# Kernel optimization log

Hardware: AMD Instinct MI355X
Metric: run time of the kernel (lower is better)

## Reference

```python
import jax, jax.numpy as jnp
import numpy as np

H = 256  # GRU hidden size


def _gru_scan(state, lengths, Wih, Whh, bih, bhh):
    # state: [B, T, D]; run a batched GRU over time, freezing h once t >= lengths[b]
    B, T, D = state.shape
    # precompute input gates for all timesteps: [T, B, 3H]
    gi_all = jnp.einsum('btd,gd->tbg', state, Wih) + bih

    def step(h, inp):
        gi, t = inp
        gh = h @ Whh.T + bhh                       # [B, 3H]
        i_r, i_z, i_n = jnp.split(gi, 3, axis=-1)
        h_r, h_z, h_n = jnp.split(gh, 3, axis=-1)
        r = jax.nn.sigmoid(i_r + h_r)
        z = jax.nn.sigmoid(i_z + h_z)
        n = jnp.tanh(i_n + r * h_n)
        h_new = (1.0 - z) * n + z * h              # torch GRUCell update
        mask = (t < lengths)[:, None]              # ragged: stop updating past length
        return jnp.where(mask, h_new, h), None

    h0 = jnp.zeros((B, H), state.dtype)
    h, _ = jax.lax.scan(step, h0, (gi_all, jnp.arange(T)))
    return h  # [B, H] = hidden after lengths[b] GRU steps


def _mlp(x, w1, b1, w2, b2, w3, b3, w4, b4, wq, bq):
    x = jax.nn.relu(x @ w1.T + b1)
    x = jax.nn.relu(x @ w2.T + b2)
    x = jax.nn.relu(x @ w3.T + b3)
    x = jax.nn.relu(x @ w4.T + b4)
    return x @ wq.T + bq  # [B, 1]


def setup_inputs() -> dict:
    key = jax.random.key(0)
    ks = jax.random.split(key, 40)
    B, T, D, A = 2048, 64, 15, 1
    inp = {}
    inp['state'] = jax.random.normal(ks[0], (B, T, D), jnp.float32)
    inp['action'] = jax.random.normal(ks[1], (B, A), jnp.float32)
    inp['lengths'] = jax.random.randint(ks[2], (B,), 1, T + 1, jnp.int32)
    i = 3
    for t in (1, 2):
        for name, shape, fan in [('Wih', (3 * H, D), D), ('Whh', (3 * H, H), H),
                                 ('bih', (3 * H,), H), ('bhh', (3 * H,), H)]:
            inp[f'g{t}_{name}'] = jax.random.normal(ks[i], shape, jnp.float32) / np.sqrt(fan)
            i += 1
        for name, (o, n) in [('fc1', (1024, H + D + A)), ('fc2', (1024, 1024)),
                             ('fc3', (512, 1024)), ('fc4', (256, 512)), ('q', (1, 256))]:
            inp[f'{name}_{t}_w'] = jax.random.normal(ks[i], (o, n), jnp.float32) / np.sqrt(n)
            i += 1
            inp[f'{name}_{t}_b'] = jax.random.normal(ks[i], (o,), jnp.float32) * 0.01
            i += 1
    return inp


def reference(state, action, lengths,
              g1_Wih, g1_Whh, g1_bih, g1_bhh,
              fc1_1_w, fc1_1_b, fc2_1_w, fc2_1_b, fc3_1_w, fc3_1_b,
              fc4_1_w, fc4_1_b, q_1_w, q_1_b,
              g2_Wih, g2_Whh, g2_bih, g2_bhh,
              fc1_2_w, fc1_2_b, fc2_2_w, fc2_2_b, fc3_2_w, fc3_2_b,
              fc4_2_w, fc4_2_b, q_2_w, q_2_b):
    h1 = _gru_scan(state, lengths, g1_Wih, g1_Whh, g1_bih, g1_bhh)
    h2 = _gru_scan(state, lengths, g2_Wih, g2_Whh, g2_bih, g2_bhh)
    aug = jnp.concatenate([state[:, 0, :], action], axis=-1)  # [B, 16]
    x1 = jnp.concatenate([aug, h1], axis=-1)                  # [B, 272]
    x2 = jnp.concatenate([aug, h2], axis=-1)
    out1 = _mlp(x1, fc1_1_w, fc1_1_b, fc2_1_w, fc2_1_b, fc3_1_w, fc3_1_b,
                fc4_1_w, fc4_1_b, q_1_w, q_1_b)
    out2 = _mlp(x2, fc1_2_w, fc1_2_b, fc2_2_w, fc2_2_b, fc3_2_w, fc3_2_b,
                fc4_2_w, fc4_2_b, q_2_w, q_2_b)
    return (out1, out2)
```

## Files before the change

### kernel.cpp

```cpp
#include <hip/hip_runtime.h>

typedef float  f32x4 __attribute__((ext_vector_type(4)));
typedef short  s16x8 __attribute__((ext_vector_type(8)));
typedef __bf16 b16x8 __attribute__((ext_vector_type(8)));

#define DEV __device__ __forceinline__

DEV unsigned short f2b(float f) {
  unsigned u = __builtin_bit_cast(unsigned, f);
  u = (u + 0x7FFFu + ((u >> 16) & 1u)) >> 16;
  return (unsigned short)u;
}
DEV float b2f(unsigned short h) {
  unsigned u = ((unsigned)h) << 16;
  return __builtin_bit_cast(float, u);
}
DEV b16x8 ld8(const unsigned short* p) {
  return __builtin_bit_cast(b16x8, *(const s16x8*)p);
}
DEV float sigm(float x) { return __builtin_amdgcn_rcpf(1.f + __expf(-x)); }
DEV float tanh_fast(float x) {
  float e = __expf(2.f * x);
  return 1.f - 2.f * __builtin_amdgcn_rcpf(e + 1.f);
}
DEV void async16(const unsigned short* g, unsigned short* l) {
  __builtin_amdgcn_global_load_lds(
      (const __attribute__((address_space(1))) unsigned int*)g,
      (__attribute__((address_space(3))) unsigned int*)l, 16, 0, 0);
}
DEV f32x4 mfma_bf16(b16x8 a, b16x8 b, f32x4 c) {
  return __builtin_amdgcn_mfma_f32_16x16x32_bf16(a, b, c, 0, 0, 0);
}

__global__ __launch_bounds__(256) void prep_waug(
    const float* __restrict__ whh0, const float* __restrict__ wih0,
    const float* __restrict__ bih0, const float* __restrict__ bhh0,
    const float* __restrict__ whh1, const float* __restrict__ wih1,
    const float* __restrict__ bih1, const float* __restrict__ bhh1,
    unsigned short* __restrict__ dst0, unsigned short* __restrict__ dst1) {
  const int g = blockIdx.y;
  const float* whh = g ? whh1 : whh0;
  const float* wih = g ? wih1 : wih0;
  const float* bih = g ? bih1 : bih0;
  const float* bhh = g ? bhh1 : bhh0;
  unsigned short* dst = g ? dst1 : dst0;
  const int i0 = blockIdx.x * 256 + threadIdx.x;
  const int stride = gridDim.x * 256;
  for (int idx = i0; idx < 768 * 288; idx += stride) {
    int j = idx / 288, k = idx - j * 288;
    float v = 0.f;
    if (k < 256)       v = whh[j * 256 + k];
    else if (k < 271)  v = wih[j * 15 + (k - 256)];
    else if (k == 271) v = (j < 512) ? (bih[j] + bhh[j]) : bih[j];
    dst[idx] = f2b(v);
  }
}

#define GRU_LDS_BYTES 140672
__global__ __launch_bounds__(512) void gru_kernel(
    const float* __restrict__ state, const float* __restrict__ action,
    const int* __restrict__ lengths,
    const unsigned short* __restrict__ waug0, const unsigned short* __restrict__ waug1,
    const float* __restrict__ bhh0, const float* __restrict__ bhh1,
    unsigned short* __restrict__ x0, unsigned short* __restrict__ x1) {
  extern __shared__ char smem[];
  unsigned short* W67L = (unsigned short*)smem;
  unsigned short* SgL  = (unsigned short*)(smem + 98304);
  unsigned short* Hb   = (unsigned short*)(smem + 131072);
  int* lenS = (int*)(smem + 140544);
  int* mlS  = (int*)(smem + 140608);
  float* tmpF = (float*)smem;

  const int tid = threadIdx.x;
  const int lane = tid & 63, w = tid >> 6;
  const int l15 = lane & 15, q = lane >> 4;
  const int g = blockIdx.x & 1;
  const int r0 = (blockIdx.x >> 1) * 16;

  const unsigned short* Waug = g ? waug1 : waug0;
  const float* bhh = g ? bhh1 : bhh0;
  unsigned short* xout = g ? x1 : x0;

  {
    const float4* src = (const float4*)(state + (size_t)r0 * 960);
    float4* dstv = (float4*)tmpF;
    for (int i = tid; i < 3840; i += 512) dstv[i] = src[i];
  }
  for (int i = tid; i < 16 * 296; i += 512) Hb[i] = 0;
  if (tid < 16) lenS[tid] = lengths[r0 + tid];
  __syncthreads();

  if (tid == 0) {
    int m = 1;
    for (int i = 0; i < 16; i++) m = lenS[i] > m ? lenS[i] : m;
    *mlS = m;
  }

  for (int s = tid; s < 64 * 32; s += 512) {
    const int t = s >> 5, L = s & 31;
    const int q2 = L >> 4, r = L & 15;
    s16x8 h;
#pragma unroll
    for (int j = 0; j < 8; j++) {
      const int k = q2 * 8 + j;
      float v = (k < 15) ? tmpF[r * 960 + t * 15 + k] : (k == 15 ? 1.0f : 0.f);
      h[j] = (short)f2b(v);
    }
    *(s16x8*)(SgL + (size_t)s * 8) = h;
  }
  __syncthreads();

  int c0[6];
  c0[0] = 32 * w;       c0[1] = 32 * w + 16;
  c0[2] = 256 + 32 * w; c0[3] = 256 + 32 * w + 16;
  c0[4] = 512 + 32 * w; c0[5] = 512 + 32 * w + 16;

  b16x8 wres[6][6];
  b16x8 waugf[6];
#pragma unroll
  for (int i = 0; i < 6; i++) {
    const unsigned short* bpi = Waug + (size_t)(c0[i] + l15) * 288 + q * 8;
#pragma unroll
    for (int j = 0; j < 6; j++) wres[i][j] = ld8(bpi + j * 32);
    waugf[i] = ld8(bpi + 256);
#pragma unroll
    for (int ks2 = 0; ks2 < 2; ks2++) {
      b16x8 v = ld8(bpi + (6 + ks2) * 32);
      *(s16x8*)(W67L + (size_t)(ks2 * 6 + i) * 4096 + tid * 8) =
          __builtin_bit_cast(s16x8, v);
    }
  }
  float bnH[2] = {bhh[c0[4] + l15], bhh[c0[5] + l15]};
  int len4[4];
#pragma unroll
  for (int r = 0; r < 4; r++) len4[r] = lenS[q * 4 + r];
  __syncthreads();
  const int maxlen = *mlS;

  float hold[2][4] = {{0, 0, 0, 0}, {0, 0, 0, 0}};
  const short qmask = (q < 2) ? (short)-1 : (short)0;
  const s16x8 qm = {qmask, qmask, qmask, qmask, qmask, qmask, qmask, qmask};

  for (int t = 0; t < maxlen; ++t) {
    __syncthreads();

    f32x4 acc[6];
#pragma unroll
    for (int i = 0; i < 6; i++) acc[i] = f32x4{0.f, 0.f, 0.f, 0.f};

    {
      s16x8 raw = *(const s16x8*)(SgL + t * 256 + ((q & 1) * 16 + l15) * 8);
      raw &= qm;
      b16x8 a8 = __builtin_bit_cast(b16x8, raw);
#pragma unroll
      for (int i = 0; i < 6; i++) acc[i] = mfma_bf16(a8, waugf[i], acc[i]);
    }
    f32x4 giN0 = acc[4], giN1 = acc[5];
    acc[4] = acc[4] + bnH[0];
    acc[5] = acc[5] + bnH[1];

#pragma unroll
    for (int j = 0; j < 6; j++) {
      b16x8 a = ld8(&Hb[l15 * 296 + j * 32 + q * 8]);
#pragma unroll
      for (int i = 0; i < 6; i++) acc[i] = mfma_bf16(a, wres[i][j], acc[i]);
    }
#pragma unroll
    for (int ks2 = 0; ks2 < 2; ks2++) {
      b16x8 a = ld8(&Hb[l15 * 296 + (6 + ks2) * 32 + q * 8]);
#pragma unroll
      for (int i = 0; i < 6; i++) {
        b16x8 bw = ld8(W67L + (size_t)(ks2 * 6 + i) * 4096 + tid * 8);
        acc[i] = mfma_bf16(a, bw, acc[i]);
      }
    }
    __syncthreads();

#pragma unroll
    for (int i = 0; i < 2; i++) {
      const int c = 32 * w + 16 * i + l15;
#pragma unroll
      for (int rg = 0; rg < 4; rg++) {
        const int row = q * 4 + rg;
        float r = sigm(acc[0 + i][rg]);
        float z = sigm(acc[2 + i][rg]);
        float inn = i ? giN1[rg] : giN0[rg];
        float hn = acc[4 + i][rg] - inn;
        float nn = tanh_fast(inn + r * hn);
        float hv = (1.f - z) * nn + z * hold[i][rg];
        hv = (t < len4[rg]) ? hv : hold[i][rg];
        hold[i][rg] = hv;
        Hb[row * 296 + c] = f2b(hv);
      }
    }
  }

#pragma unroll
  for (int i = 0; i < 2; i++) {
    const int c = 32 * w + 16 * i + l15;
#pragma unroll
    for (int rg = 0; rg < 4; rg++) {
      const int row = q * 4 + rg;
      xout[(size_t)(r0 + row) * 288 + 16 + c] = f2b(hold[i][rg]);
    }
  }
  {
    const int row = tid >> 5, cc = tid & 31;
    float v; int col;
    if (cc < 15)       { v = state[(size_t)(r0 + row) * 960 + cc]; col = cc; }
    else if (cc == 15) { v = action[r0 + row]; col = 15; }
    else               { v = 0.f; col = 256 + cc; }
    xout[(size_t)(r0 + row) * 288 + col] = f2b(v);
  }
}

template <int BM, int BN>
__global__ __launch_bounds__(256, 2) void gemm_bias_relu(
    const unsigned short* __restrict__ A0, const unsigned short* __restrict__ A1,
    const float* __restrict__ W0, const float* __restrict__ W1,
    const float* __restrict__ b0, const float* __restrict__ b1,
    unsigned short* __restrict__ Y0, unsigned short* __restrict__ Y1,
    int N, int K, int Ksrc) {
  const unsigned short* A = blockIdx.z ? A1 : A0;
  const float* W = blockIdx.z ? W1 : W0;
  const float* bias = blockIdx.z ? b1 : b0;
  unsigned short* Y = blockIdx.z ? Y1 : Y0;

  constexpr int MT = BM / 32;
  constexpr int NT = BN / 32;
  const int tid = threadIdx.x;
  const int lane = tid & 63, wid = tid >> 6;
  const int wm = wid >> 1, wn = wid & 1;
  const int l15 = lane & 15, q = lane >> 4;
  const int m0 = blockIdx.x * BM, n0 = blockIdx.y * BN;

  __shared__ unsigned short As[BM * 32];
  __shared__ unsigned short Bs[BN * 32];

  f32x4 acc[MT][NT];
#pragma unroll
  for (int mi = 0; mi < MT; mi++)
#pragma unroll
    for (int ni = 0; ni < NT; ni++) acc[mi][ni] = f32x4{0.f, 0.f, 0.f, 0.f};

  const int srow = tid >> 2, scol = (tid & 3) * 8;

  for (int k0 = 0; k0 < K; k0 += 32) {
#pragma unroll
    for (int g64 = 0; g64 < BM / 64; g64++)
      async16(A + (size_t)(m0 + g64 * 64 + srow) * K + scol + k0,
              &As[g64 * 2048 + tid * 8]);
#pragma unroll
    for (int g64 = 0; g64 < BN / 64; g64++) {
      const int wr = n0 + g64 * 64 + srow;
      const int k = k0 + scol;
      s16x8 h = {0, 0, 0, 0, 0, 0, 0, 0};
      if (k < Ksrc) {
        const float* wp = W + (size_t)wr * Ksrc + k;
        const float4 f0 = *(const float4*)wp;
        const float4 f1 = *(const float4*)(wp + 4);
        h[0] = (short)f2b(f0.x); h[1] = (short)f2b(f0.y);
        h[2] = (short)f2b(f0.z); h[3] = (short)f2b(f0.w);
        h[4] = (short)f2b(f1.x); h[5] = (short)f2b(f1.y);
        h[6] = (short)f2b(f1.z); h[7] = (short)f2b(f1.w);
      }
      *(s16x8*)&Bs[g64 * 2048 + tid * 8] = h;
    }
    __syncthreads();

    b16x8 af[MT], bf[NT];
#pragma unroll
    for (int mi = 0; mi < MT; mi++)
      af[mi] = ld8(&As[(wm * (BM / 2) + mi * 16 + l15) * 32 + q * 8]);
#pragma unroll
    for (int ni = 0; ni < NT; ni++)
      bf[ni] = ld8(&Bs[(wn * (BN / 2) + ni * 16 + l15) * 32 + q * 8]);
#pragma unroll
    for (int mi = 0; mi < MT; mi++)
#pragma unroll
      for (int ni = 0; ni < NT; ni++)
        acc[mi][ni] = mfma_bf16(af[mi], bf[ni], acc[mi][ni]);
    __syncthreads();
  }

#pragma unroll
  for (int ni = 0; ni < NT; ni++) {
    const int col = n0 + wn * (BN / 2) + ni * 16 + l15;
    const float bv = bias[col];
#pragma unroll
    for (int mi = 0; mi < MT; mi++) {
      const int rbase = m0 + wm * (BM / 2) + mi * 16 + q * 4;
#pragma unroll
      for (int rg = 0; rg < 4; rg++) {
        float v = acc[mi][ni][rg] + bv;
        v = fmaxf(v, 0.f);
        Y[(size_t)(rbase + rg) * N + col] = f2b(v);
      }
    }
  }
}

__global__ __launch_bounds__(256) void qdot(
    const unsigned short* __restrict__ y0, const unsigned short* __restrict__ y1,
    const float* __restrict__ qw0, const float* __restrict__ qb0,
    const float* __restrict__ qw1, const float* __restrict__ qb1,
    float* __restrict__ out) {
  const int lane = threadIdx.x & 63, wid = threadIdx.x >> 6;
  const int row = blockIdx.x * 4 + wid;
  const int br = blockIdx.y;
  const unsigned short* y = br ? y1 : y0;
  const float* qw = br ? qw1 : qw0;
  const float* qb = br ? qb1 : qb0;
  const unsigned short* p = y + (size_t)row * 256 + lane * 4;
  float s = 0.f;
#pragma unroll
  for (int j = 0; j < 4; j++) s += b2f(p[j]) * qw[lane * 4 + j];
#pragma unroll
  for (int off = 32; off > 0; off >>= 1) s += __shfl_down(s, off);
  if (lane == 0) out[br * 2048 + row] = s + qb[0];
}

extern "C" void kernel_launch(void* const* d_in, const int* in_sizes, int n_in,
                              void* d_out, int out_size, void* d_ws, size_t ws_size,
                              hipStream_t stream) {
  const float* state   = (const float*)d_in[0];
  const float* action  = (const float*)d_in[1];
  const int*   lengths = (const int*)d_in[2];
  const float* g_wih[2] = {(const float*)d_in[3], (const float*)d_in[17]};
  const float* g_whh[2] = {(const float*)d_in[4], (const float*)d_in[18]};
  const float* g_bih[2] = {(const float*)d_in[5], (const float*)d_in[19]};
  const float* g_bhh[2] = {(const float*)d_in[6], (const float*)d_in[20]};
  const float* fcw[2][4] = {
      {(const float*)d_in[7], (const float*)d_in[9], (const float*)d_in[11], (const float*)d_in[13]},
      {(const float*)d_in[21], (const float*)d_in[23], (const float*)d_in[25], (const float*)d_in[27]}};
  const float* fcb[2][4] = {
      {(const float*)d_in[8], (const float*)d_in[10], (const float*)d_in[12], (const float*)d_in[14]},
      {(const float*)d_in[22], (const float*)d_in[24], (const float*)d_in[26], (const float*)d_in[28]}};
  const float* qw[2] = {(const float*)d_in[15], (const float*)d_in[29]};
  const float* qb[2] = {(const float*)d_in[16], (const float*)d_in[30]};
  float* out = (float*)d_out;

  uintptr_t base = (uintptr_t)d_ws;
  auto alloc = [&](size_t bytes) -> unsigned short* {
    void* p = (void*)base;
    base += (bytes + 255) & ~(size_t)255;
    return (unsigned short*)p;
  };
  unsigned short *waug[2], *xb[2], *yA[2], *yB[2];
  for (int g = 0; g < 2; g++) waug[g] = alloc(768 * 288 * 2);
  for (int g = 0; g < 2; g++) xb[g] = alloc(2048 * 288 * 2);
  for (int g = 0; g < 2; g++) yA[g] = alloc(2048 * 1024 * 2);
  for (int g = 0; g < 2; g++) yB[g] = alloc(2048 * 1024 * 2);
  (void)ws_size; (void)in_sizes; (void)n_in; (void)out_size;

  prep_waug<<<dim3(32, 2), 256, 0, stream>>>(
      g_whh[0], g_wih[0], g_bih[0], g_bhh[0],
      g_whh[1], g_wih[1], g_bih[1], g_bhh[1], waug[0], waug[1]);

  static bool attr_done = false;
  hipFuncSetAttribute((const void*)gru_kernel,
                      hipFuncAttributeMaxDynamicSharedMemorySize, GRU_LDS_BYTES);
  (void)attr_done;

  gru_kernel<<<dim3(256), dim3(512), GRU_LDS_BYTES, stream>>>(
      state, action, lengths, waug[0], waug[1], g_bhh[0], g_bhh[1], xb[0], xb[1]);

  gemm_bias_relu<64, 128><<<dim3(32, 8, 2), 256, 0, stream>>>(
      xb[0], xb[1], fcw[0][0], fcw[1][0], fcb[0][0], fcb[1][0], yA[0], yA[1],
      1024, 288, 272);
  gemm_bias_relu<64, 128><<<dim3(32, 8, 2), 256, 0, stream>>>(
      yA[0], yA[1], fcw[0][1], fcw[1][1], fcb[0][1], fcb[1][1], yB[0], yB[1],
      1024, 1024, 1024);
  gemm_bias_relu<64, 64><<<dim3(32, 8, 2), 256, 0, stream>>>(
      yB[0], yB[1], fcw[0][2], fcw[1][2], fcb[0][2], fcb[1][2], yA[0], yA[1],
      512, 1024, 1024);
  gemm_bias_relu<64, 64><<<dim3(32, 4, 2), 256, 0, stream>>>(
      yA[0], yA[1], fcw[0][3], fcw[1][3], fcb[0][3], fcb[1][3], yB[0], yB[1],
      256, 512, 512);

  qdot<<<dim3(512, 2), 256, 0, stream>>>(yB[0], yB[1], qw[0], qb[0], qw[1], qb[1], out);
}
```

Baseline: 355.9 us.

## Pre-convert MLP weights to bf16, fuse fc4 with q head, double-buffer GRU hidden state

A single prep kernel now converts all MLP weights to bf16 once, so the GEMMs can load W with async global-to-LDS copies instead of converting fp32 on the fly. It also initialises the output with the q bias. The GRU kernel gets a double-buffered, XOR-swizzled packed hidden-state buffer, which removes one barrier per timestep and reduces LDS bank conflicts. The GEMM tiles grow to 128 rows, and fc4 is fused with the q dot product using atomicAdd reductions, which drops the separate qdot kernel. The cost is extra weight-conversion traffic on every call and accumulation order that depends on atomics.

```diff
diff --git a/kernel.cpp b/kernel.cpp
--- a/kernel.cpp
+++ b/kernel.cpp
@@ -11,10 +11,6 @@
   u = (u + 0x7FFFu + ((u >> 16) & 1u)) >> 16;
   return (unsigned short)u;
 }
-DEV float b2f(unsigned short h) {
-  unsigned u = ((unsigned)h) << 16;
-  return __builtin_bit_cast(float, u);
-}
 DEV b16x8 ld8(const unsigned short* p) {
   return __builtin_bit_cast(b16x8, *(const s16x8*)p);
 }
@@ -32,31 +28,55 @@
   return __builtin_amdgcn_mfma_f32_16x16x32_bf16(a, b, c, 0, 0, 0);
 }
 
-__global__ __launch_bounds__(256) void prep_waug(
-    const float* __restrict__ whh0, const float* __restrict__ wih0,
-    const float* __restrict__ bih0, const float* __restrict__ bhh0,
-    const float* __restrict__ whh1, const float* __restrict__ wih1,
-    const float* __restrict__ bih1, const float* __restrict__ bhh1,
-    unsigned short* __restrict__ dst0, unsigned short* __restrict__ dst1) {
-  const int g = blockIdx.y;
-  const float* whh = g ? whh1 : whh0;
-  const float* wih = g ? wih1 : wih0;
-  const float* bih = g ? bih1 : bih0;
-  const float* bhh = g ? bhh1 : bhh0;
-  unsigned short* dst = g ? dst1 : dst0;
+struct PrepArgs {
+  const float *whh[2], *wih[2], *bih[2], *bhh[2];
+  const float *src[2][4];
+  unsigned short *waug[2], *dst[2][4];
+  const float *qb[2];
+  float *out;
+};
+
+__global__ __launch_bounds__(256) void prep_kernel(PrepArgs p) {
+  const int job = blockIdx.y;
   const int i0 = blockIdx.x * 256 + threadIdx.x;
   const int stride = gridDim.x * 256;
-  for (int idx = i0; idx < 768 * 288; idx += stride) {
-    int j = idx / 288, k = idx - j * 288;
-    float v = 0.f;
-    if (k < 256)       v = whh[j * 256 + k];
-    else if (k < 271)  v = wih[j * 15 + (k - 256)];
-    else if (k == 271) v = (j < 512) ? (bih[j] + bhh[j]) : bih[j];
-    dst[idx] = f2b(v);
-  }
-}
-
-#define GRU_LDS_BYTES 140672
+  if (job < 2) {
+    const float* whh = p.whh[job];
+    const float* wih = p.wih[job];
+    const float* bih = p.bih[job];
+    const float* bhh = p.bhh[job];
+    unsigned short* dst = p.waug[job];
+    for (int idx = i0; idx < 768 * 288; idx += stride) {
+      int j = idx / 288, k = idx - j * 288;
+      float v = 0.f;
+      if (k < 256) {
+        int o = k & 31;
+        int kk = (k & 0x1E0) + (o >> 1) + ((o & 1) << 4);
+        v = whh[j * 256 + kk];
+      } else if (k < 271)  v = wih[j * 15 + (k - 256)];
+      else if (k == 271)   v = (j < 512) ? (bih[j] + bhh[j]) : bih[j];
+      dst[idx] = f2b(v);
+    }
+  } else if (job < 10) {
+    const int jj = job - 2, br = jj >> 2, ly = jj & 3;
+    const int rowsA[4] = {1024, 1024, 512, 256};
+    const int scA[4]   = {272, 1024, 1024, 512};
+    const int dcA[4]   = {288, 1024, 1024, 512};
+    const float* src = p.src[br][ly];
+    unsigned short* dst = p.dst[br][ly];
+    const int sc = scA[ly], dc = dcA[ly], tot = rowsA[ly] * dc;
+    for (int idx = i0; idx < tot; idx += stride) {
+      int r = idx / dc, c = idx - r * dc;
+      float v = (c < sc) ? src[r * sc + c] : 0.f;
+      dst[idx] = f2b(v);
+    }
+  } else {
+    for (int idx = i0; idx < 4096; idx += stride)
+      p.out[idx] = p.qb[idx >> 11][0];
+  }
+}
+
+#define GRU_LDS_BYTES 147584
 __global__ __launch_bounds__(512) void gru_kernel(
     const float* __restrict__ state, const float* __restrict__ action,
     const int* __restrict__ lengths,
@@ -66,9 +86,9 @@
   extern __shared__ char smem[];
   unsigned short* W67L = (unsigned short*)smem;
   unsigned short* SgL  = (unsigned short*)(smem + 98304);
-  unsigned short* Hb   = (unsigned short*)(smem + 131072);
-  int* lenS = (int*)(smem + 140544);
-  int* mlS  = (int*)(smem + 140608);
+  unsigned*       Hb2  = (unsigned*)(smem + 131072);
+  int* lenS = (int*)(smem + 147456);
+  int* mlS  = (int*)(smem + 147520);
   float* tmpF = (float*)smem;
 
   const int tid = threadIdx.x;
@@ -86,10 +106,9 @@
     float4* dstv = (float4*)tmpF;
     for (int i = tid; i < 3840; i += 512) dstv[i] = src[i];
   }
-  for (int i = tid; i < 16 * 296; i += 512) Hb[i] = 0;
+  for (int i = tid; i < 4096; i += 512) Hb2[i] = 0;
   if (tid < 16) lenS[tid] = lengths[r0 + tid];
   __syncthreads();
-
   if (tid == 0) {
     int m = 1;
     for (int i = 0; i < 16; i++) m = lenS[i] > m ? lenS[i] : m;
@@ -134,12 +153,29 @@
   int len4[4];
 #pragma unroll
   for (int r = 0; r < 4; r++) len4[r] = lenS[q * 4 + r];
+
+  int aOff[8];
+#pragma unroll
+  for (int j = 0; j < 8; j++) {
+    const int cj = 4 * j + q;
+    const int pj = (cj & 24) | ((cj & 7) ^ (l15 & 7));
+    aOff[j] = l15 * 128 + pj * 4;
+  }
+  int wOff[4];
+#pragma unroll
+  for (int rg = 0; rg < 4; rg++) {
+    const int row = q * 4 + rg;
+    const int cb = 4 * w + (l15 >> 2);
+    const int pw = (cb & 24) | ((cb & 7) ^ (row & 7));
+    wOff[rg] = row * 128 + pw * 4 + (l15 & 3);
+  }
   __syncthreads();
   const int maxlen = *mlS;
 
   float hold[2][4] = {{0, 0, 0, 0}, {0, 0, 0, 0}};
   const short qmask = (q < 2) ? (short)-1 : (short)0;
   const s16x8 qm = {qmask, qmask, qmask, qmask, qmask, qmask, qmask, qmask};
+  int poff = 0;
 
   for (int t = 0; t < maxlen; ++t) {
     __syncthreads();
@@ -159,40 +195,42 @@
     acc[4] = acc[4] + bnH[0];
     acc[5] = acc[5] + bnH[1];
 
+    const unsigned* hb = Hb2 + poff;
 #pragma unroll
     for (int j = 0; j < 6; j++) {
-      b16x8 a = ld8(&Hb[l15 * 296 + j * 32 + q * 8]);
+      b16x8 a = __builtin_bit_cast(b16x8, *(const uint4*)(hb + aOff[j]));
 #pragma unroll
       for (int i = 0; i < 6; i++) acc[i] = mfma_bf16(a, wres[i][j], acc[i]);
     }
 #pragma unroll
     for (int ks2 = 0; ks2 < 2; ks2++) {
-      b16x8 a = ld8(&Hb[l15 * 296 + (6 + ks2) * 32 + q * 8]);
+      b16x8 a = __builtin_bit_cast(b16x8, *(const uint4*)(hb + aOff[6 + ks2]));
 #pragma unroll
       for (int i = 0; i < 6; i++) {
         b16x8 bw = ld8(W67L + (size_t)(ks2 * 6 + i) * 4096 + tid * 8);
         acc[i] = mfma_bf16(a, bw, acc[i]);
       }
     }
-    __syncthreads();
-
-#pragma unroll
-    for (int i = 0; i < 2; i++) {
-      const int c = 32 * w + 16 * i + l15;
-#pragma unroll
-      for (int rg = 0; rg < 4; rg++) {
-        const int row = q * 4 + rg;
-        float r = sigm(acc[0 + i][rg]);
-        float z = sigm(acc[2 + i][rg]);
-        float inn = i ? giN1[rg] : giN0[rg];
-        float hn = acc[4 + i][rg] - inn;
-        float nn = tanh_fast(inn + r * hn);
-        float hv = (1.f - z) * nn + z * hold[i][rg];
-        hv = (t < len4[rg]) ? hv : hold[i][rg];
-        hold[i][rg] = hv;
-        Hb[row * 296 + c] = f2b(hv);
-      }
-    }
+
+    unsigned* hbw = Hb2 + (poff ^ 2048);
+#pragma unroll
+    for (int rg = 0; rg < 4; rg++) {
+      const bool live = (t < len4[rg]);
+      float r0g = sigm(acc[0][rg]);
+      float z0 = sigm(acc[2][rg]);
+      float n0 = tanh_fast(giN0[rg] + r0g * (acc[4][rg] - giN0[rg]));
+      float h0 = n0 + z0 * (hold[0][rg] - n0);
+      h0 = live ? h0 : hold[0][rg];
+      hold[0][rg] = h0;
+      float r1g = sigm(acc[1][rg]);
+      float z1 = sigm(acc[3][rg]);
+      float n1 = tanh_fast(giN1[rg] + r1g * (acc[5][rg] - giN1[rg]));
+      float h1 = n1 + z1 * (hold[1][rg] - n1);
+      h1 = live ? h1 : hold[1][rg];
+      hold[1][rg] = h1;
+      hbw[wOff[rg]] = (unsigned)f2b(h0) | ((unsigned)f2b(h1) << 16);
+    }
+    poff ^= 2048;
   }
 
 #pragma unroll
@@ -217,12 +255,12 @@
 template <int BM, int BN>
 __global__ __launch_bounds__(256, 2) void gemm_bias_relu(
     const unsigned short* __restrict__ A0, const unsigned short* __restrict__ A1,
-    const float* __restrict__ W0, const float* __restrict__ W1,
+    const unsigned short* __restrict__ W0, const unsigned short* __restrict__ W1,
     const float* __restrict__ b0, const float* __restrict__ b1,
     unsigned short* __restrict__ Y0, unsigned short* __restrict__ Y1,
-    int N, int K, int Ksrc) {
+    int N, int K) {
   const unsigned short* A = blockIdx.z ? A1 : A0;
-  const float* W = blockIdx.z ? W1 : W0;
+  const unsigned short* W = blockIdx.z ? W1 : W0;
   const float* bias = blockIdx.z ? b1 : b0;
   unsigned short* Y = blockIdx.z ? Y1 : Y0;
 
@@ -251,21 +289,9 @@
       async16(A + (size_t)(m0 + g64 * 64 + srow) * K + scol + k0,
               &As[g64 * 2048 + tid * 8]);
 #pragma unroll
-    for (int g64 = 0; g64 < BN / 64; g64++) {
-      const int wr = n0 + g64 * 64 + srow;
-      const int k = k0 + scol;
-      s16x8 h = {0, 0, 0, 0, 0, 0, 0, 0};
-      if (k < Ksrc) {
-        const float* wp = W + (size_t)wr * Ksrc + k;
-        const float4 f0 = *(const float4*)wp;
-        const float4 f1 = *(const float4*)(wp + 4);
-        h[0] = (short)f2b(f0.x); h[1] = (short)f2b(f0.y);
-        h[2] = (short)f2b(f0.z); h[3] = (short)f2b(f0.w);
-        h[4] = (short)f2b(f1.x); h[5] = (short)f2b(f1.y);
-        h[6] = (short)f2b(f1.z); h[7] = (short)f2b(f1.w);
-      }
-      *(s16x8*)&Bs[g64 * 2048 + tid * 8] = h;
-    }
+    for (int g64 = 0; g64 < BN / 64; g64++)
+      async16(W + (size_t)(n0 + g64 * 64 + srow) * K + scol + k0,
+              &Bs[g64 * 2048 + tid * 8]);
     __syncthreads();
 
     b16x8 af[MT], bf[NT];
@@ -300,24 +326,80 @@
   }
 }
 
-__global__ __launch_bounds__(256) void qdot(
-    const unsigned short* __restrict__ y0, const unsigned short* __restrict__ y1,
-    const float* __restrict__ qw0, const float* __restrict__ qb0,
-    const float* __restrict__ qw1, const float* __restrict__ qb1,
+__global__ __launch_bounds__(256, 2) void fc4q_kernel(
+    const unsigned short* __restrict__ A0, const unsigned short* __restrict__ A1,
+    const unsigned short* __restrict__ W0, const unsigned short* __restrict__ W1,
+    const float* __restrict__ b0, const float* __restrict__ b1,
+    const float* __restrict__ qw0, const float* __restrict__ qw1,
     float* __restrict__ out) {
-  const int lane = threadIdx.x & 63, wid = threadIdx.x >> 6;
-  const int row = blockIdx.x * 4 + wid;
-  const int br = blockIdx.y;
-  const unsigned short* y = br ? y1 : y0;
-  const float* qw = br ? qw1 : qw0;
-  const float* qb = br ? qb1 : qb0;
-  const unsigned short* p = y + (size_t)row * 256 + lane * 4;
-  float s = 0.f;
-#pragma unroll
-  for (int j = 0; j < 4; j++) s += b2f(p[j]) * qw[lane * 4 + j];
-#pragma unroll
-  for (int off = 32; off > 0; off >>= 1) s += __shfl_down(s, off);
-  if (lane == 0) out[br * 2048 + row] = s + qb[0];
+  const unsigned short* A = blockIdx.z ? A1 : A0;
+  const unsigned short* W = blockIdx.z ? W1 : W0;
+  const float* bias = blockIdx.z ? b1 : b0;
+  const float* qw = blockIdx.z ? qw1 : qw0;
+
+  const int tid = threadIdx.x;
+  const int lane = tid & 63, wn = tid >> 6;
+  const int l15 = lane & 15, q = lane >> 4;
+  const int m0 = blockIdx.x * 32;
+  const int nbase = blockIdx.y * 128;
+  const int K = 512;
+
+  __shared__ unsigned short As[32 * 32];
+  __shared__ unsigned short Bs[128 * 32];
+  __shared__ float red[32][4];
+
+  f32x4 acc[2][2];
+#pragma unroll
+  for (int mi = 0; mi < 2; mi++)
+#pragma unroll
+    for (int ni = 0; ni < 2; ni++) acc[mi][ni] = f32x4{0.f, 0.f, 0.f, 0.f};
+
+  const int srow = tid >> 2, scol = (tid & 3) * 8;
+  for (int k0 = 0; k0 < K; k0 += 32) {
+    if (tid < 128)
+      async16(A + (size_t)(m0 + srow) * K + scol + k0, &As[tid * 8]);
+#pragma unroll
+    for (int g64 = 0; g64 < 2; g64++)
+      async16(W + (size_t)(nbase + g64 * 64 + srow) * K + scol + k0,
+              &Bs[g64 * 2048 + tid * 8]);
+    __syncthreads();
+
+    b16x8 af[2], bf[2];
+#pragma unroll
+    for (int mi = 0; mi < 2; mi++)
+      af[mi] = ld8(&As[(mi * 16 + l15) * 32 + q * 8]);
+#pragma unroll
+    for (int ni = 0; ni < 2; ni++)
+      bf[ni] = ld8(&Bs[(wn * 32 + ni * 16 + l15) * 32 + q * 8]);
+#pragma unroll
+    for (int mi = 0; mi < 2; mi++)
+#pragma unroll
+      for (int ni = 0; ni < 2; ni++)
+        acc[mi][ni] = mfma_bf16(af[mi], bf[ni], acc[mi][ni]);
+    __syncthreads();
+  }
+
+#pragma unroll
+  for (int mi = 0; mi < 2; mi++) {
+#pragma unroll
+    for (int rg = 0; rg < 4; rg++) {
+      float s = 0.f;
+#pragma unroll
+      for (int ni = 0; ni < 2; ni++) {
+        const int col = nbase + wn * 32 + ni * 16 + l15;
+        float v = fmaxf(acc[mi][ni][rg] + bias[col], 0.f);
+        s += v * qw[col];
+      }
+#pragma unroll
+      for (int off = 1; off < 16; off <<= 1) s += __shfl_xor(s, off);
+      if (l15 == 0) red[mi * 16 + q * 4 + rg][wn] = s;
+    }
+  }
+  __syncthreads();
+  if (tid < 32) {
+    float t = red[tid][0] + red[tid][1] + red[tid][2] + red[tid][3];
+    atomicAdd(out + (size_t)blockIdx.z * 2048 + m0 + tid, t);
+  }
 }
 
 extern "C" void kernel_launch(void* const* d_in, const int* in_sizes, int n_in,
@@ -346,37 +428,43 @@
     base += (bytes + 255) & ~(size_t)255;
     return (unsigned short*)p;
   };
-  unsigned short *waug[2], *xb[2], *yA[2], *yB[2];
+  unsigned short *waug[2], *w1b[2], *w2b[2], *w3b[2], *w4b[2], *xb[2], *yA[2], *yB[2];
   for (int g = 0; g < 2; g++) waug[g] = alloc(768 * 288 * 2);
+  for (int g = 0; g < 2; g++) w1b[g] = alloc(1024 * 288 * 2);
+  for (int g = 0; g < 2; g++) w2b[g] = alloc(1024 * 1024 * 2);
+  for (int g = 0; g < 2; g++) w3b[g] = alloc(512 * 1024 * 2);
+  for (int g = 0; g < 2; g++) w4b[g] = alloc(256 * 512 * 2);
   for (int g = 0; g < 2; g++) xb[g] = alloc(2048 * 288 * 2);
   for (int g = 0; g < 2; g++) yA[g] = alloc(2048 * 1024 * 2);
   for (int g = 0; g < 2; g++) yB[g] = alloc(2048 * 1024 * 2);
   (void)ws_size; (void)in_sizes; (void)n_in; (void)out_size;
 
-  prep_waug<<<dim3(32, 2), 256, 0, stream>>>(
-      g_whh[0], g_wih[0], g_bih[0], g_bhh[0],
-      g_whh[1], g_wih[1], g_bih[1], g_bhh[1], waug[0], waug[1]);
-
-  static bool attr_done = false;
-  hipFuncSetAttribute((const void*)gru_kernel,
-                      hipFuncAttributeMaxDynamicSharedMemorySize, GRU_LDS_BYTES);
-  (void)attr_done;
-
+  PrepArgs pa;
+  for (int g = 0; g < 2; g++) {
+    pa.whh[g] = g_whh[g]; pa.wih[g] = g_wih[g];
+    pa.bih[g] = g_bih[g]; pa.bhh[g] = g_bhh[g];
+    pa.waug[g] = waug[g];
+    pa.src[g][0] = fcw[g][0]; pa.dst[g][0] = w1b[g];
+    pa.src[g][1] = fcw[g][1]; pa.dst[g][1] = w2b[g];
+    pa.src[g][2] = fcw[g][2]; pa.dst[g][2] = w3b[g];
+    pa.src[g][3] = fcw[g][3]; pa.dst[g][3] = w4b[g];
+    pa.qb[g] = qb[g];
+  }
+  pa.out = out;
+  prep_kernel<<<dim3(64, 11), 256, 0, stream>>>(pa);
+
+  (void)hipFuncSetAttribute((const void*)gru_kernel,
+                            hipFuncAttributeMaxDynamicSharedMemorySize,
+                            GRU_LDS_BYTES);
   gru_kernel<<<dim3(256), dim3(512), GRU_LDS_BYTES, stream>>>(
       state, action, lengths, waug[0], waug[1], g_bhh[0], g_bhh[1], xb[0], xb[1]);
 
-  gemm_bias_relu<64, 128><<<dim3(32, 8, 2), 256, 0, stream>>>(
-      xb[0], xb[1], fcw[0][0], fcw[1][0], fcb[0][0], fcb[1][0], yA[0], yA[1],
-      1024, 288, 272);
-  gemm_bias_relu<64, 128><<<dim3(32, 8, 2), 256, 0, stream>>>(
-      yA[0], yA[1], fcw[0][1], fcw[1][1], fcb[0][1], fcb[1][1], yB[0], yB[1],
-      1024, 1024, 1024);
-  gemm_bias_relu<64, 64><<<dim3(32, 8, 2), 256, 0, stream>>>(
-      yB[0], yB[1], fcw[0][2], fcw[1][2], fcb[0][2], fcb[1][2], yA[0], yA[1],
-      512, 1024, 1024);
-  gemm_bias_relu<64, 64><<<dim3(32, 4, 2), 256, 0, stream>>>(
-      yA[0], yA[1], fcw[0][3], fcw[1][3], fcb[0][3], fcb[1][3], yB[0], yB[1],
-      256, 512, 512);
-
-  qdot<<<dim3(512, 2), 256, 0, stream>>>(yB[0], yB[1], qw[0], qb[0], qw[1], qb[1], out);
-}
+  gemm_bias_relu<128, 128><<<dim3(16, 8, 2), 256, 0, stream>>>(
+      xb[0], xb[1], w1b[0], w1b[1], fcb[0][0], fcb[1][0], yA[0], yA[1], 1024, 288);
+  gemm_bias_relu<128, 128><<<dim3(16, 8, 2), 256, 0, stream>>>(
+      yA[0], yA[1], w2b[0], w2b[1], fcb[0][1], fcb[1][1], yB[0], yB[1], 1024, 1024);
+  gemm_bias_relu<128, 64><<<dim3(16, 8, 2), 256, 0, stream>>>(
+      yB[0], yB[1], w3b[0], w3b[1], fcb[0][2], fcb[1][2], yA[0], yA[1], 512, 1024);
+  fc4q_kernel<<<dim3(64, 2, 2), 256, 0, stream>>>(
+      yA[0], yA[1], w4b[0], w4b[1], fcb[0][3], fcb[1][3], qw[0], qw[1], out);
+}
```

Measured after the change: 336.8 us. -5.4%, faster.
